# Optimization experiments

Hardware: AMD Instinct MI355X
Metric: run time of the kernel (lower is better)

## Reference

```python
import jax, jax.numpy as jnp
import numpy as np

GRID = 64
NPTS = 2048
EPS = 1e-5


def gridding_reverse(grid3):
    # grid3: [B,S,S,S] occupancy grid -> point cloud [B,S^3,3] in [-1,1];
    # each vertex is the weight-averaged position of its 8 adjacent cells, zero if empty.
    B, S = grid3.shape[0], grid3.shape[1]
    g = jnp.pad(grid3, ((0, 0), (1, 0), (1, 0), (1, 0)))
    ax = jnp.arange(S, dtype=grid3.dtype)
    cx, cy, cz = jnp.meshgrid(ax, ax, ax, indexing='ij')
    base = jnp.stack([cx, cy, cz], axis=-1)  # [S,S,S,3]
    wsum = jnp.zeros((B, S, S, S), grid3.dtype)
    pos = jnp.zeros((B, S, S, S, 3), grid3.dtype)
    for dx in (0, 1):
        for dy in (0, 1):
            for dz in (0, 1):
                w = g[:, dx:dx + S, dy:dy + S, dz:dz + S]
                off = jnp.asarray([dx - 1.0, dy - 1.0, dz - 1.0], grid3.dtype)
                pos = pos + w[..., None] * (base + off)
                wsum = wsum + w
    avg = pos / jnp.maximum(wsum, 1e-8)[..., None]
    pt = avg / (S * 0.5) - 1.0
    pt = jnp.where((wsum > 0)[..., None], pt, 0.0)
    return pt.reshape(B, S * S * S, 3)


def maxpool3d(x, k):
    return jax.lax.reduce_window(x, -jnp.inf, jax.lax.max, (1, 1, k, k, k), (1, 1, k, k, k), 'VALID')


def random_point_sampling(cloud, noise, n_points):
    # uniformly pick n_points among points with nonzero coord-sum (random-score top-k
    # replaces torch.randperm per sample; fixed output shape, jit-safe)
    mask = jnp.sum(cloud, axis=2) != 0
    scores = jnp.where(mask, noise, -1e30)
    idx = jax.lax.top_k(scores, n_points)[1]  # [B,n_points]
    return jnp.take_along_axis(cloud, idx[..., None], axis=1)


def cubic_feature_sampling(pt, feat):
    # pt [B,N,3] in [-1,1]; feat [B,C,S,S,S] -> [B,N,8*C]: features at the 8 corners
    # of the cell containing each point.
    B, C, S = feat.shape[0], feat.shape[1], feat.shape[2]
    featf = jnp.transpose(feat.reshape(B, C, S * S * S), (0, 2, 1))  # [B,S^3,C]
    lo = jnp.floor((pt + 1.0) * (0.5 * S)).astype(jnp.int32)  # lower corner index
    outs = []
    for dx in (0, 1):
        for dy in (0, 1):
            for dz in (0, 1):
                ix = jnp.clip(lo[..., 0] + dx, 0, S - 1)
                iy = jnp.clip(lo[..., 1] + dy, 0, S - 1)
                iz = jnp.clip(lo[..., 2] + dz, 0, S - 1)
                lin = (ix * S + iy) * S + iz  # [B,N]
                outs.append(jnp.take_along_axis(featf, lin[..., None], axis=1))
    return jnp.concatenate(outs, axis=-1)  # [B,N,8C]


def conv1d(x, w, b):
    y = jax.lax.conv_general_dilated(x, w, (1,), [(1, 1)], dimension_numbers=('NCH', 'OIH', 'NCH'))
    return y + b[None, :, None]


def bn1d(x, g, b, m, v):
    inv = jax.lax.rsqrt(v + EPS) * g
    return x * inv[None, :, None] + (b - m * inv)[None, :, None]


def setup_inputs():
    key = jax.random.key(0)
    ks = jax.random.split(key, 32)
    B = 8

    def nrm(k, shape, fan):
        return (jax.random.normal(k, shape, jnp.float32) / np.sqrt(fan)).astype(jnp.float32)

    inp = {
        'data': jax.random.normal(ks[0], (B, 1, GRID, GRID, GRID), jnp.float32),
        'skip_32': jax.random.normal(ks[1], (B, 32, 32, 32, 32), jnp.float32),
        'skip_16': jax.random.normal(ks[2], (B, 64, 16, 16, 16), jnp.float32),
        'skip_8': jax.random.normal(ks[3], (B, 128, 8, 8, 8), jnp.float32),
        'noise': jax.random.normal(ks[4], (B, 4096), jnp.float32),
        'w11': nrm(ks[5], (1792, 1792), 1792), 'b11': jnp.zeros(1792, jnp.float32),
        'w12': nrm(ks[6], (1792, 448), 1792), 'b12': jnp.zeros(448, jnp.float32),
        'w13': nrm(ks[7], (448, 100), 448), 'b13': jnp.zeros(100, jnp.float32),
        'c1w': nrm(ks[8], (1024, 2048, 3), 2048 * 3), 'c1b': jnp.zeros(1024, jnp.float32),
        'g1': jnp.ones(1024, jnp.float32), 'be1': jnp.zeros(1024, jnp.float32),
        'm1': 0.01 * jax.random.normal(ks[9], (1024,), jnp.float32),
        'v1': 1.0 + 0.1 * jax.random.uniform(ks[10], (1024,), jnp.float32),
        'c2w': nrm(ks[11], (512, 1024, 3), 1024 * 3), 'c2b': jnp.zeros(512, jnp.float32),
        'g2': jnp.ones(512, jnp.float32), 'be2': jnp.zeros(512, jnp.float32),
        'm2': 0.01 * jax.random.normal(ks[12], (512,), jnp.float32),
        'v2': 1.0 + 0.1 * jax.random.uniform(ks[13], (512,), jnp.float32),
        'c3w': nrm(ks[14], (128, 512, 3), 512 * 3), 'c3b': jnp.zeros(128, jnp.float32),
        'g3': jnp.ones(128, jnp.float32), 'be3': jnp.zeros(128, jnp.float32),
        'm3': 0.01 * jax.random.normal(ks[15], (128,), jnp.float32),
        'v3': 1.0 + 0.1 * jax.random.uniform(ks[16], (128,), jnp.float32),
        'c4w': nrm(ks[17], (32, 128, 3), 128 * 3), 'c4b': jnp.zeros(32, jnp.float32),
        'g4': jnp.ones(32, jnp.float32), 'be4': jnp.zeros(32, jnp.float32),
        'm4': 0.01 * jax.random.normal(ks[18], (32,), jnp.float32),
        'v4': 1.0 + 0.1 * jax.random.uniform(ks[19], (32,), jnp.float32),
        'w15a': nrm(ks[20], (3200, 512), 3200), 'b15a': jnp.zeros(512, jnp.float32),
        'w15b': nrm(ks[21], (512, 128), 512), 'b15b': jnp.zeros(128, jnp.float32),
        'w15c': nrm(ks[22], (128, 15), 128), 'b15c': jnp.zeros(15, jnp.float32),
    }
    return inp


def reference(data, skip_32, skip_16, skip_8, noise,
              w11, b11, w12, b12, w13, b13,
              c1w, c1b, g1, be1, m1, v1,
              c2w, c2b, g2, be2, m2, v2,
              c3w, c3b, g3, be3, m3, v3,
              c4w, c4b, g4, be4, m4, v4,
              w15a, b15a, w15b, b15b, w15c, b15c):
    B = data.shape[0]
    completion = (jnp.abs(data) <= 1.0).astype(jnp.float32)  # [B,1,64,64,64]
    pt = gridding_reverse(completion[:, 0])                  # [B,64^3,3]
    x = pt.reshape(B, 3, GRID, GRID, GRID)                   # raw reshape as in source
    x = maxpool3d(x, 4)                                      # [B,3,16,16,16]
    cloud = x.reshape(B, 4096, 3)
    cloud = random_point_sampling(cloud, noise, NPTS)        # [B,2048,3]
    f = jnp.concatenate([
        cubic_feature_sampling(cloud, skip_32),              # [B,2048,256]
        cubic_feature_sampling(cloud, skip_16),              # [B,2048,512]
        cubic_feature_sampling(cloud, skip_8)], axis=2)      # [B,2048,1792]
    f = jax.nn.relu(f @ w11 + b11)
    f = jax.nn.relu(f @ w12 + b12)
    f = jax.nn.relu(f @ w13 + b13)                           # [B,2048,100]
    y = jax.nn.relu(bn1d(conv1d(f, c1w, c1b), g1, be1, m1, v1))
    y = jax.nn.relu(bn1d(conv1d(y, c2w, c2b), g2, be2, m2, v2))
    y = jax.nn.relu(bn1d(conv1d(y, c3w, c3b), g3, be3, m3, v3))
    y = jax.nn.relu(bn1d(conv1d(y, c4w, c4b), g4, be4, m4, v4))  # [B,32,100]
    h = y.reshape(B, -1)                                     # [B,3200]
    h = jax.nn.relu(h @ w15a + b15a)                         # dropout = identity (eval)
    h = jax.nn.relu(h @ w15b + b15b)
    return h @ w15c + b15c                                   # [B,15]
```

## Files before the change

### kernel.cpp

```cpp
#include <hip/hip_runtime.h>
#include <cstdint>

#define S64 64
#define S3 (S64*S64*S64)
#define NB 8
#define NPTS 2048

typedef unsigned short ushort_t;
typedef __attribute__((ext_vector_type(8))) short bh8;
typedef __attribute__((ext_vector_type(4))) float f4v;

__device__ inline ushort_t bf_rne(float a) {
    unsigned u = __float_as_uint(a);
    unsigned r = (u + 0x7FFFu + ((u >> 16) & 1u)) >> 16;
    return (ushort_t)r;
}
__device__ inline void split2(float a, ushort_t& h, ushort_t& lo) {
    h = bf_rne(a);
    float hf = __uint_as_float(((unsigned)h) << 16);
    lo = bf_rne(a - hf);
}

__global__ void k_gridding(const float* __restrict__ data, float* __restrict__ pt_buf) {
    int idx = blockIdx.x * blockDim.x + threadIdx.x;
    if (idx >= NB * S3) return;
    int b = idx / S3;
    int cell = idx - b * S3;
    int i = cell >> 12;
    int j = (cell >> 6) & 63;
    int k = cell & 63;
    const float* db = data + (size_t)b * S3;
    float wsum = 0.f, px = 0.f, py = 0.f, pz = 0.f;
#pragma unroll
    for (int dx = 0; dx < 2; ++dx)
#pragma unroll
    for (int dy = 0; dy < 2; ++dy)
#pragma unroll
    for (int dz = 0; dz < 2; ++dz) {
        int xi = i + dx - 1, yj = j + dy - 1, zk = k + dz - 1;
        float w = 0.f;
        if (xi >= 0 && yj >= 0 && zk >= 0) {
            float v = db[((xi << 6) + yj << 6) + zk];
            w = (fabsf(v) <= 1.0f) ? 1.0f : 0.0f;
        }
        px += w * (float)xi;
        py += w * (float)yj;
        pz += w * (float)zk;
        wsum += w;
    }
    float wc = fmaxf(wsum, 1e-8f);
    float ptx = (px / wc) / 32.0f - 1.0f;
    float pty = (py / wc) / 32.0f - 1.0f;
    float ptz = (pz / wc) / 32.0f - 1.0f;
    if (!(wsum > 0.f)) { ptx = 0.f; pty = 0.f; ptz = 0.f; }
    float* o = pt_buf + (size_t)b * (S3 * 3) + (size_t)cell * 3;
    o[0] = ptx; o[1] = pty; o[2] = ptz;
}

__global__ void k_maxpool(const float* __restrict__ pt_buf, float* __restrict__ pooled) {
    int idx = blockIdx.x * blockDim.x + threadIdx.x;
    if (idx >= NB * 12288) return;
    int b = idx / 12288;
    int r = idx - b * 12288;
    int c = r >> 12;
    int r2 = r & 4095;
    int X = r2 >> 8;
    int Y = (r2 >> 4) & 15;
    int Z = r2 & 15;
    const float* src = pt_buf + (size_t)b * (S3 * 3) + (size_t)c * S3;
    float m = -INFINITY;
#pragma unroll
    for (int u = 0; u < 4; ++u)
#pragma unroll
    for (int v = 0; v < 4; ++v)
#pragma unroll
    for (int w = 0; w < 4; ++w) {
        float val = src[((4 * X + u) << 12) + ((4 * Y + v) << 6) + (4 * Z + w)];
        m = fmaxf(m, val);
    }
    pooled[idx] = m;
}

__global__ void k_topk(const float* __restrict__ pooled, const float* __restrict__ noise,
                       float* __restrict__ sc) {
    __shared__ unsigned long long keys[4096];
    int b = blockIdx.x;
    int tid = threadIdx.x;
    for (int p = tid; p < 4096; p += 1024) {
        const float* cp = pooled + (size_t)b * 12288 + (size_t)p * 3;
        float ssum = (cp[0] + cp[1]) + cp[2];
        float score = (ssum != 0.0f) ? noise[b * 4096 + p] : -1e30f;
        unsigned int u = __float_as_uint(score);
        unsigned int s = (u & 0x80000000u) ? ~u : (u | 0x80000000u);
        keys[p] = ((unsigned long long)(~s) << 32) | (unsigned int)p;
    }
    __syncthreads();
    for (int k = 2; k <= 4096; k <<= 1) {
        for (int j = k >> 1; j > 0; j >>= 1) {
            for (int t = tid; t < 4096; t += 1024) {
                int ixj = t ^ j;
                if (ixj > t) {
                    bool up = ((t & k) == 0);
                    unsigned long long a = keys[t], c = keys[ixj];
                    if (up ? (a > c) : (a < c)) { keys[t] = c; keys[ixj] = a; }
                }
            }
            __syncthreads();
        }
    }
    for (int r = tid; r < NPTS; r += 1024) {
        int p = (int)(keys[r] & 0xFFFFFFFFu);
        const float* cp = pooled + (size_t)b * 12288 + (size_t)p * 3;
        float* o = sc + ((size_t)b * NPTS + r) * 3;
        o[0] = cp[0]; o[1] = cp[1]; o[2] = cp[2];
    }
}

__global__ void k_cubic(const float* __restrict__ sc,
                        const float* __restrict__ s32,
                        const float* __restrict__ s16,
                        const float* __restrict__ s8,
                        ushort_t* __restrict__ Ap, int row0) {
    int rl = blockIdx.y;
    int row = row0 + rl;
    int col = blockIdx.x * 256 + threadIdx.x;
    int b = row >> 11;
    const float* p = sc + (size_t)row * 3;
    float ptx = p[0], pty = p[1], ptz = p[2];
    const float* feat;
    int S, c, q;
    if (col < 256)      { S = 32; q = col >> 5;  c = col & 31;
                          feat = s32 + (size_t)b * 32 * 32768; }
    else if (col < 768) { int cc = col - 256; S = 16; q = cc >> 6; c = cc & 63;
                          feat = s16 + (size_t)b * 64 * 4096; }
    else                { int cc = col - 768; S = 8;  q = cc >> 7; c = cc & 127;
                          feat = s8 + (size_t)b * 128 * 512; }
    int dx = (q >> 2) & 1, dy = (q >> 1) & 1, dz = q & 1;
    float half = 0.5f * (float)S;
    int lx = (int)floorf((ptx + 1.0f) * half);
    int ly = (int)floorf((pty + 1.0f) * half);
    int lz = (int)floorf((ptz + 1.0f) * half);
    int ix = min(max(lx + dx, 0), S - 1);
    int iy = min(max(ly + dy, 0), S - 1);
    int iz = min(max(lz + dz, 0), S - 1);
    int lin = (ix * S + iy) * S + iz;
    float v = feat[(size_t)c * S * S * S + lin];
    ushort_t h, lo; split2(v, h, lo);
    size_t base = (size_t)rl * 5376 + 3 * (size_t)col;
    Ap[base] = h; Ap[base + 1] = h; Ap[base + 2] = lo;
}

__global__ void k_split_transpose(const float* __restrict__ W, ushort_t* __restrict__ Bp,
                                  int K, int N, int Npad) {
    __shared__ float t[32][33];
    int tx = threadIdx.x, ty = threadIdx.y;
    int n0 = blockIdx.x * 32, k0 = blockIdx.y * 32;
#pragma unroll
    for (int kk = 0; kk < 4; ++kk) {
        int k = k0 + ty + kk * 8, n = n0 + tx;
        float v = (k < K && n < N) ? W[(size_t)k * N + n] : 0.f;
        t[ty + kk * 8][tx] = v;
    }
    __syncthreads();
    size_t Kp = 3 * (size_t)K;
#pragma unroll
    for (int nn = 0; nn < 4; ++nn) {
        int n = n0 + ty + nn * 8;
        int k = k0 + tx;
        if (n >= Npad || k >= K) continue;
        float a = t[tx][ty + nn * 8];
        ushort_t h, lo; split2(a, h, lo);
        size_t base = (size_t)n * Kp + 3 * (size_t)k;
        Bp[base] = h; Bp[base + 1] = lo; Bp[base + 2] = h;
    }
}

__global__ void k_split_rows_b(const float* __restrict__ src, ushort_t* __restrict__ dst, int K) {
    int r = blockIdx.y;
    int k = blockIdx.x * 256 + threadIdx.x;
    if (k >= K) return;
    float a = src[(size_t)r * K + k];
    ushort_t h, lo; split2(a, h, lo);
    size_t base = (size_t)r * (3 * (size_t)K) + 3 * (size_t)k;
    dst[base] = h; dst[base + 1] = lo; dst[base + 2] = h;
}

__global__ void k_split_im2col(const float* __restrict__ src, ushort_t* __restrict__ Ap,
                               int Cin, int Kin) {
    int mp = blockIdx.y;
    int k = blockIdx.x * 256 + threadIdx.x;
    if (k >= Kin) return;
    float v = 0.f;
    if (mp < 800) {
        int b = mp / 100, h = mp - b * 100;
        int c = k / 3, t = k - c * 3;
        int hh = h + t - 1;
        if (hh >= 0 && hh < 100)
            v = src[((size_t)b * Cin + c) * 100 + hh];
    }
    ushort_t h16, lo; split2(v, h16, lo);
    size_t base = (size_t)mp * (3 * (size_t)Kin) + 3 * (size_t)k;
    Ap[base] = h16; Ap[base + 1] = h16; Ap[base + 2] = lo;
}

__global__ void k_zero(float* __restrict__ p, int n) {
    int i = blockIdx.x * 256 + threadIdx.x;
    if (i < n) p[i] = 0.f;
}

__global__ void k_epi(const float* __restrict__ acc, const float* __restrict__ bias,
                      const float* __restrict__ bn_g, const float* __restrict__ bn_b,
                      const float* __restrict__ bn_m, const float* __restrict__ bn_v,
                      float* __restrict__ Cf, ushort_t* __restrict__ Cs,
                      int M, int N, int ldc, int relu, int dobn, int mode) {
    int idx = blockIdx.x * 256 + threadIdx.x;
    if (idx >= M * N) return;
    int m = idx / N, n = idx - m * N;
    float v = acc[idx] + bias[n];
    if (dobn) {
        float inv = rsqrtf(bn_v[n] + 1e-5f) * bn_g[n];
        v = v * inv + (bn_b[n] - bn_m[n] * inv);
    }
    if (relu) v = fmaxf(v, 0.f);
    if (mode == 0) {
        Cf[idx] = v;
    } else if (mode == 1) {
        int b = m / 100, h = m - b * 100;
        Cf[((size_t)b * N + n) * 100 + h] = v;
    } else {
        ushort_t h, lo; split2(v, h, lo);
        size_t base = (size_t)m * ldc + 3 * (size_t)n;
        Cs[base] = h; Cs[base + 1] = h; Cs[base + 2] = lo;
    }
}

#define GLDS(g, s) __builtin_amdgcn_global_load_lds( \
    (const __attribute__((address_space(1))) void*)(g), \
    (__attribute__((address_space(3))) void*)(s), 16, 0, 0)

__global__ __launch_bounds__(256) void k_gemm_mfma(
    const ushort_t* __restrict__ Ap, const ushort_t* __restrict__ Bp,
    const float* __restrict__ bias,
    const float* __restrict__ bn_g, const float* __restrict__ bn_b,
    const float* __restrict__ bn_m, const float* __restrict__ bn_v,
    float* __restrict__ Cf, ushort_t* __restrict__ Cs,
    int M, int N, int Kp, int ldc,
    int relu, int dobn, int omode, int osplit,
    int ks, int Kc)
{
    __shared__ short As[2][128][32];
    __shared__ short Bs[2][128][32];
    int tid = threadIdx.x;
    int l = tid & 63, w = tid >> 6;
    int wr = w >> 1, wc = w & 1;
    int m0 = blockIdx.y * 128, n0 = blockIdx.x * 128;
    int kbeg = blockIdx.z * Kc;

    f4v acc[4][4];
#pragma unroll
    for (int i = 0; i < 4; ++i)
#pragma unroll
        for (int j = 0; j < 4; ++j) acc[i][j] = (f4v){0.f, 0.f, 0.f, 0.f};

    int lr = l >> 2;
    int lc = l & 3;
    int lcs = lc ^ ((lr >> 2) & 3);
    const ushort_t* pa0 = Ap + (size_t)(m0 + w * 32 + lr) * Kp + lcs * 8 + kbeg;
    const ushort_t* pa1 = pa0 + (size_t)16 * Kp;
    const ushort_t* pb0 = Bp + (size_t)(n0 + w * 32 + lr) * Kp + lcs * 8 + kbeg;
    const ushort_t* pb1 = pb0 + (size_t)16 * Kp;

    int fr = l & 15;
    int ko = ((l >> 4) ^ ((fr >> 2) & 3)) * 8;
    int nt = Kc >> 5;

    GLDS(pa0, &As[0][w * 32][0]);
    GLDS(pa1, &As[0][w * 32 + 16][0]);
    GLDS(pb0, &Bs[0][w * 32][0]);
    GLDS(pb1, &Bs[0][w * 32 + 16][0]);
    __syncthreads();

    for (int t = 0; t < nt; ++t) {
        int cur = t & 1;
        if (t + 1 < nt) {
            int ko2 = (t + 1) << 5;
            GLDS(pa0 + ko2, &As[cur ^ 1][w * 32][0]);
            GLDS(pa1 + ko2, &As[cur ^ 1][w * 32 + 16][0]);
            GLDS(pb0 + ko2, &Bs[cur ^ 1][w * 32][0]);
            GLDS(pb1 + ko2, &Bs[cur ^ 1][w * 32 + 16][0]);
        }
        bh8 af[4], bfr[4];
#pragma unroll
        for (int i = 0; i < 4; ++i)
            af[i] = *reinterpret_cast<const bh8*>(&As[cur][wr * 64 + i * 16 + fr][ko]);
#pragma unroll
        for (int j = 0; j < 4; ++j)
            bfr[j] = *reinterpret_cast<const bh8*>(&Bs[cur][wc * 64 + j * 16 + fr][ko]);
#pragma unroll
        for (int i = 0; i < 4; ++i)
#pragma unroll
            for (int j = 0; j < 4; ++j)
                acc[i][j] = __builtin_amdgcn_mfma_f32_16x16x32_bf16(af[i], bfr[j], acc[i][j], 0, 0, 0);
        __syncthreads();
    }

#pragma unroll
    for (int i = 0; i < 4; ++i)
#pragma unroll
        for (int j = 0; j < 4; ++j) {
#pragma unroll
            for (int r = 0; r < 4; ++r) {
                int m = m0 + wr * 64 + i * 16 + (l >> 4) * 4 + r;
                int n = n0 + wc * 64 + j * 16 + fr;
                if (m >= M || n >= N) continue;
                if (ks > 1) {
                    atomicAdd(&Cf[(size_t)m * N + n], acc[i][j][r]);
                    continue;
                }
                float v = acc[i][j][r] + bias[n];
                if (dobn) {
                    float inv = rsqrtf(bn_v[n] + 1e-5f) * bn_g[n];
                    v = v * inv + (bn_b[n] - bn_m[n] * inv);
                }
                if (relu) v = fmaxf(v, 0.f);
                if (osplit) {
                    ushort_t h, lo; split2(v, h, lo);
                    size_t base = (size_t)m * ldc + 3 * (size_t)n;
                    Cs[base] = h; Cs[base + 1] = h; Cs[base + 2] = lo;
                } else if (omode == 0) {
                    Cf[(size_t)m * N + n] = v;
                } else {
                    int bb = m / 100, h = m - bb * 100;
                    Cf[((size_t)bb * N + n) * 100 + h] = v;
                }
            }
        }
}

__global__ __launch_bounds__(256) void k_skinny2(
    const float* __restrict__ A, const float* __restrict__ B,
    float* __restrict__ Cacc, int M, int N, int K, int Kc)
{
    int lane = threadIdx.x & 63;
    int wv = threadIdx.x >> 6;
    int n = blockIdx.x * 64 + lane;
    int m = blockIdx.y * 4 + wv;
    if (m >= M || n >= N) return;
    int kbeg = blockIdx.z * Kc;
    int kend = min(K, kbeg + Kc);
    const float* a = A + (size_t)m * K;
    const float* b = B + n;
    float acc = 0.f;
#pragma unroll 4
    for (int k = kbeg; k < kend; ++k)
        acc = fmaf(a[k], b[(size_t)k * N], acc);
    atomicAdd(&Cacc[(size_t)m * N + n], acc);
}

extern "C" void kernel_launch(void* const* d_in, const int* in_sizes, int n_in,
                              void* d_out, int out_size, void* d_ws, size_t ws_size,
                              hipStream_t stream) {
    const float* data  = (const float*)d_in[0];
    const float* s32   = (const float*)d_in[1];
    const float* s16   = (const float*)d_in[2];
    const float* s8    = (const float*)d_in[3];
    const float* noise = (const float*)d_in[4];
    const float* w11 = (const float*)d_in[5];  const float* b11 = (const float*)d_in[6];
    const float* w12 = (const float*)d_in[7];  const float* b12 = (const float*)d_in[8];
    const float* w13 = (const float*)d_in[9];  const float* b13 = (const float*)d_in[10];
    const float* c1w = (const float*)d_in[11]; const float* c1b = (const float*)d_in[12];
    const float* g1 = (const float*)d_in[13];  const float* be1 = (const float*)d_in[14];
    const float* m1 = (const float*)d_in[15];  const float* v1  = (const float*)d_in[16];
    const float* c2w = (const float*)d_in[17]; const float* c2b = (const float*)d_in[18];
    const float* g2 = (const float*)d_in[19];  const float* be2 = (const float*)d_in[20];
    const float* m2 = (const float*)d_in[21];  const float* v2  = (const float*)d_in[22];
    const float* c3w = (const float*)d_in[23]; const float* c3b = (const float*)d_in[24];
    const float* g3 = (const float*)d_in[25];  const float* be3 = (const float*)d_in[26];
    const float* m3 = (const float*)d_in[27];  const float* v3  = (const float*)d_in[28];
    const float* c4w = (const float*)d_in[29]; const float* c4b = (const float*)d_in[30];
    const float* g4 = (const float*)d_in[31];  const float* be4 = (const float*)d_in[32];
    const float* m4 = (const float*)d_in[33];  const float* v4  = (const float*)d_in[34];
    const float* w15a = (const float*)d_in[35]; const float* b15a = (const float*)d_in[36];
    const float* w15b = (const float*)d_in[37]; const float* b15b = (const float*)d_in[38];
    const float* w15c = (const float*)d_in[39]; const float* b15c = (const float*)d_in[40];
    float* out = (float*)d_out;
    (void)in_sizes; (void)n_in; (void)out_size;

    char* ws = (char*)d_ws;

    size_t offs[16];
    auto plan = [&](size_t P, size_t* o) -> size_t {
        size_t off = 0;
        auto al = [&](size_t b) { size_t x = off; off += (b + 255) & ~(size_t)255; return x; };
        o[0]  = al(P * 5376 * 2);
        o[1]  = al(P * 5376 * 2);
        o[2]  = al(P * 1344 * 2);
        o[3]  = al((size_t)1792 * 5376 * 2);
        o[4]  = al((size_t)512 * 5376 * 2);
        o[5]  = al((size_t)128 * 1344 * 2);
        o[6]  = al(P * 448 * 4);
        o[7]  = al((size_t)16384 * 100 * 4);
        o[8]  = al((size_t)NB * 1024 * 100 * 4);
        o[9]  = al((size_t)NB * 512 * 100 * 4);
        o[10] = al((size_t)NB * 128 * 100 * 4);
        o[11] = al((size_t)NB * 32 * 100 * 4);
        o[12] = al(NB * 12288 * 4);
        o[13] = al(NB * NPTS * 3 * 4);
        o[14] = al(NB * 512 * 4);
        o[15] = al(NB * 128 * 4);
        return off;
    };
    size_t P = 8192;
    if (plan(P, offs) > ws_size) P = 4096;
    plan(P, offs);
    int nparts = (int)(16384 / P);
    int Pb = (int)(P / 128);
    int ksFC2 = (P == 8192) ? 2 : 4;
    int KcFC2 = 5376 / ksFC2;

    float*    pt_buf = (float*)(ws + offs[0]);
    ushort_t* Aq     = (ushort_t*)(ws + offs[0]);
    ushort_t* Aconv  = (ushort_t*)(ws + offs[0]);
    ushort_t* Fq     = (ushort_t*)(ws + offs[1]);
    ushort_t* Bconv  = (ushort_t*)(ws + offs[1]);
    ushort_t* Gq     = (ushort_t*)(ws + offs[2]);
    ushort_t* Bp1    = (ushort_t*)(ws + offs[3]);
    ushort_t* Bp2    = (ushort_t*)(ws + offs[4]);
    ushort_t* Bp3    = (ushort_t*)(ws + offs[5]);
    float*    Cacc   = (float*)(ws + offs[6]);
    float* f4     = (float*)(ws + offs[7]);
    float* y1     = (float*)(ws + offs[8]);
    float* y2     = (float*)(ws + offs[9]);
    float* y3     = (float*)(ws + offs[10]);
    float* y4     = (float*)(ws + offs[11]);
    float* pooled = (float*)(ws + offs[12]);
    float* scb    = (float*)(ws + offs[13]);
    float* h2     = (float*)(ws + offs[14]);
    float* h3     = (float*)(ws + offs[15]);

    k_gridding<<<(NB * S3 + 255) / 256, 256, 0, stream>>>(data, pt_buf);
    k_maxpool<<<(NB * 12288 + 255) / 256, 256, 0, stream>>>(pt_buf, pooled);
    k_topk<<<NB, 1024, 0, stream>>>(pooled, noise, scb);

    k_split_transpose<<<dim3(56, 56), dim3(32, 8), 0, stream>>>(w11, Bp1, 1792, 1792, 1792);
    k_split_transpose<<<dim3(16, 56), dim3(32, 8), 0, stream>>>(w12, Bp2, 1792, 448, 512);
    k_split_transpose<<<dim3(4, 14),  dim3(32, 8), 0, stream>>>(w13, Bp3, 448, 100, 128);

    for (int q = 0; q < nparts; ++q) {
        k_cubic<<<dim3(7, (unsigned)P), 256, 0, stream>>>(scb, s32, s16, s8, Aq, q * (int)P);
        k_gemm_mfma<<<dim3(14, Pb), 256, 0, stream>>>(Aq, Bp1, b11,
            nullptr, nullptr, nullptr, nullptr, nullptr, Fq,
            (int)P, 1792, 5376, 5376, 1, 0, 0, 1, 1, 5376);
        k_zero<<<((int)P * 448 + 255) / 256, 256, 0, stream>>>(Cacc, (int)P * 448);
        k_gemm_mfma<<<dim3(4, Pb, ksFC2), 256, 0, stream>>>(Fq, Bp2, nullptr,
            nullptr, nullptr, nullptr, nullptr, Cacc, nullptr,
            (int)P, 448, 5376, 0, 0, 0, 0, 0, ksFC2, KcFC2);
        k_epi<<<((int)P * 448 + 255) / 256, 256, 0, stream>>>(Cacc, b12,
            nullptr, nullptr, nullptr, nullptr, nullptr, Gq,
            (int)P, 448, 1344, 1, 0, 2);
        k_zero<<<((int)P * 100 + 255) / 256, 256, 0, stream>>>(Cacc, (int)P * 100);
        k_gemm_mfma<<<dim3(1, Pb, 6), 256, 0, stream>>>(Gq, Bp3, nullptr,
            nullptr, nullptr, nullptr, nullptr, Cacc, nullptr,
            (int)P, 100, 1344, 0, 0, 0, 0, 0, 6, 224);
        k_epi<<<((int)P * 100 + 255) / 256, 256, 0, stream>>>(Cacc, b13,
            nullptr, nullptr, nullptr, nullptr, f4 + (size_t)q * P * 100, nullptr,
            (int)P, 100, 0, 1, 0, 0);
    }

    k_split_im2col<<<dim3(24, 896), 256, 0, stream>>>(f4, Aconv, 2048, 6144);
    k_split_rows_b<<<dim3(24, 1024), 256, 0, stream>>>(c1w, Bconv, 6144);
    k_zero<<<(800 * 1024 + 255) / 256, 256, 0, stream>>>(Cacc, 800 * 1024);
    k_gemm_mfma<<<dim3(8, 7, 8), 256, 0, stream>>>(Aconv, Bconv, nullptr,
        nullptr, nullptr, nullptr, nullptr, Cacc, nullptr,
        800, 1024, 18432, 0, 0, 0, 0, 0, 8, 2304);
    k_epi<<<(800 * 1024 + 255) / 256, 256, 0, stream>>>(Cacc, c1b,
        g1, be1, m1, v1, y1, nullptr, 800, 1024, 0, 1, 1, 1);

    k_split_im2col<<<dim3(12, 896), 256, 0, stream>>>(y1, Aconv, 1024, 3072);
    k_split_rows_b<<<dim3(12, 512), 256, 0, stream>>>(c2w, Bconv, 3072);
    k_zero<<<(800 * 512 + 255) / 256, 256, 0, stream>>>(Cacc, 800 * 512);
    k_gemm_mfma<<<dim3(4, 7, 8), 256, 0, stream>>>(Aconv, Bconv, nullptr,
        nullptr, nullptr, nullptr, nullptr, Cacc, nullptr,
        800, 512, 9216, 0, 0, 0, 0, 0, 8, 1152);
    k_epi<<<(800 * 512 + 255) / 256, 256, 0, stream>>>(Cacc, c2b,
        g2, be2, m2, v2, y2, nullptr, 800, 512, 0, 1, 1, 1);

    k_split_im2col<<<dim3(6, 896), 256, 0, stream>>>(y2, Aconv, 512, 1536);
    k_split_rows_b<<<dim3(6, 128), 256, 0, stream>>>(c3w, Bconv, 1536);
    k_zero<<<(800 * 128 + 255) / 256, 256, 0, stream>>>(Cacc, 800 * 128);
    k_gemm_mfma<<<dim3(1, 7, 16), 256, 0, stream>>>(Aconv, Bconv, nullptr,
        nullptr, nullptr, nullptr, nullptr, Cacc, nullptr,
        800, 128, 4608, 0, 0, 0, 0, 0, 16, 288);
    k_epi<<<(800 * 128 + 255) / 256, 256, 0, stream>>>(Cacc, c3b,
        g3, be3, m3, v3, y3, nullptr, 800, 128, 0, 1, 1, 1);

    k_split_im2col<<<dim3(2, 896), 256, 0, stream>>>(y3, Aconv, 128, 384);
    k_split_rows_b<<<dim3(2, 32), 256, 0, stream>>>(c4w, Bconv, 384);
    k_zero<<<(800 * 32 + 255) / 256, 256, 0, stream>>>(Cacc, 800 * 32);
    k_gemm_mfma<<<dim3(1, 7, 6), 256, 0, stream>>>(Aconv, Bconv, nullptr,
        nullptr, nullptr, nullptr, nullptr, Cacc, nullptr,
        800, 32, 1152, 0, 0, 0, 0, 0, 6, 192);
    k_epi<<<(800 * 32 + 255) / 256, 256, 0, stream>>>(Cacc, c4b,
        g4, be4, m4, v4, y4, nullptr, 800, 32, 0, 1, 1, 1);

    k_zero<<<(8 * 512 + 255) / 256, 256, 0, stream>>>(Cacc, 8 * 512);
    k_skinny2<<<dim3(8, 2, 32), 256, 0, stream>>>(y4, w15a, Cacc, 8, 512, 3200, 100);
    k_epi<<<(8 * 512 + 255) / 256, 256, 0, stream>>>(Cacc, b15a,
        nullptr, nullptr, nullptr, nullptr, h2, nullptr, 8, 512, 0, 1, 0, 0);
    k_zero<<<(8 * 128 + 255) / 256, 256, 0, stream>>>(Cacc, 8 * 128);
    k_skinny2<<<dim3(2, 2, 8), 256, 0, stream>>>(h2, w15b, Cacc, 8, 128, 512, 64);
    k_epi<<<(8 * 128 + 255) / 256, 256, 0, stream>>>(Cacc, b15b,
        nullptr, nullptr, nullptr, nullptr, h3, nullptr, 8, 128, 0, 1, 0, 0);
    k_zero<<<(8 * 15 + 255) / 256, 256, 0, stream>>>(Cacc, 8 * 15);
    k_skinny2<<<dim3(1, 2, 2), 256, 0, stream>>>(h3, w15c, Cacc, 8, 15, 128, 64);
    k_epi<<<(8 * 15 + 255) / 256, 256, 0, stream>>>(Cacc, b15c,
        nullptr, nullptr, nullptr, nullptr, out, nullptr, 8, 15, 0, 0, 0, 0);
}
```

Before: 1.452 ms.

## Triple-buffer GEMM LDS tiles with explicit vmcnt waits and drop swizzle

Moves the MFMA GEMM from double to triple LDS buffering, prefetching two K-tiles ahead. Explicit s_waitcnt vmcnt(4) plus a raw s_barrier replace __syncthreads, so the next tile's async global-to-LDS loads can stay in flight across the barrier. It also removes the XOR swizzle on LDS column placement, which may bring back LDS bank conflicts on the fragment reads. LDS use per block grows by half, which may lower occupancy.

```diff
diff --git a/kernel.cpp b/kernel.cpp
--- a/kernel.cpp
+++ b/kernel.cpp
@@ -248,8 +248,8 @@
     int relu, int dobn, int omode, int osplit,
     int ks, int Kc)
 {
-    __shared__ short As[2][128][32];
-    __shared__ short Bs[2][128][32];
+    __shared__ short As[3][128][32];
+    __shared__ short Bs[3][128][32];
     int tid = threadIdx.x;
     int l = tid & 63, w = tid >> 6;
     int wr = w >> 1, wc = w & 1;
@@ -264,45 +264,56 @@
 
     int lr = l >> 2;
     int lc = l & 3;
-    int lcs = lc ^ ((lr >> 2) & 3);
-    const ushort_t* pa0 = Ap + (size_t)(m0 + w * 32 + lr) * Kp + lcs * 8 + kbeg;
+    const ushort_t* pa0 = Ap + (size_t)(m0 + w * 32 + lr) * Kp + lc * 8 + kbeg;
     const ushort_t* pa1 = pa0 + (size_t)16 * Kp;
-    const ushort_t* pb0 = Bp + (size_t)(n0 + w * 32 + lr) * Kp + lcs * 8 + kbeg;
+    const ushort_t* pb0 = Bp + (size_t)(n0 + w * 32 + lr) * Kp + lc * 8 + kbeg;
     const ushort_t* pb1 = pb0 + (size_t)16 * Kp;
 
     int fr = l & 15;
-    int ko = ((l >> 4) ^ ((fr >> 2) & 3)) * 8;
+    int ko = (l >> 4) * 8;
     int nt = Kc >> 5;
 
-    GLDS(pa0, &As[0][w * 32][0]);
-    GLDS(pa1, &As[0][w * 32 + 16][0]);
-    GLDS(pb0, &Bs[0][w * 32][0]);
-    GLDS(pb1, &Bs[0][w * 32 + 16][0]);
-    __syncthreads();
-
+#define STAGE(bi, t) do { int _o = (t) << 5;               \
+        GLDS(pa0 + _o, &As[bi][w * 32][0]);                \
+        GLDS(pa1 + _o, &As[bi][w * 32 + 16][0]);           \
+        GLDS(pb0 + _o, &Bs[bi][w * 32][0]);                \
+        GLDS(pb1 + _o, &Bs[bi][w * 32 + 16][0]); } while (0)
+
+    STAGE(0, 0);
+    if (nt > 1) {
+        STAGE(1, 1);
+        asm volatile("s_waitcnt vmcnt(4) lgkmcnt(0)" ::: "memory");
+    } else {
+        asm volatile("s_waitcnt vmcnt(0) lgkmcnt(0)" ::: "memory");
+    }
+    __builtin_amdgcn_s_barrier();
+    asm volatile("" ::: "memory");
+
+    int bi = 0;
     for (int t = 0; t < nt; ++t) {
-        int cur = t & 1;
-        if (t + 1 < nt) {
-            int ko2 = (t + 1) << 5;
-            GLDS(pa0 + ko2, &As[cur ^ 1][w * 32][0]);
-            GLDS(pa1 + ko2, &As[cur ^ 1][w * 32 + 16][0]);
-            GLDS(pb0 + ko2, &Bs[cur ^ 1][w * 32][0]);
-            GLDS(pb1 + ko2, &Bs[cur ^ 1][w * 32 + 16][0]);
-        }
+        int b2 = bi + 2; if (b2 >= 3) b2 -= 3;
+        if (t + 2 < nt) STAGE(b2, t + 2);
         bh8 af[4], bfr[4];
 #pragma unroll
         for (int i = 0; i < 4; ++i)
-            af[i] = *reinterpret_cast<const bh8*>(&As[cur][wr * 64 + i * 16 + fr][ko]);
+            af[i] = *reinterpret_cast<const bh8*>(&As[bi][wr * 64 + i * 16 + fr][ko]);
 #pragma unroll
         for (int j = 0; j < 4; ++j)
-            bfr[j] = *reinterpret_cast<const bh8*>(&Bs[cur][wc * 64 + j * 16 + fr][ko]);
+            bfr[j] = *reinterpret_cast<const bh8*>(&Bs[bi][wc * 64 + j * 16 + fr][ko]);
 #pragma unroll
         for (int i = 0; i < 4; ++i)
 #pragma unroll
             for (int j = 0; j < 4; ++j)
                 acc[i][j] = __builtin_amdgcn_mfma_f32_16x16x32_bf16(af[i], bfr[j], acc[i][j], 0, 0, 0);
-        __syncthreads();
-    }
+        if (t + 1 < nt) {
+            if (t + 2 < nt) asm volatile("s_waitcnt vmcnt(4) lgkmcnt(0)" ::: "memory");
+            else            asm volatile("s_waitcnt vmcnt(0) lgkmcnt(0)" ::: "memory");
+            __builtin_amdgcn_s_barrier();
+            asm volatile("" ::: "memory");
+        }
+        bi = (bi + 1 == 3) ? 0 : bi + 1;
+    }
+#undef STAGE
 
 #pragma unroll
     for (int i = 0; i < 4; ++i)
```

After: 1.469 ms. Within noise of the previous version (+1.2%).
